# Performance work log

Hardware: AMD Instinct MI355X
Metric: run time of the kernel (lower is better)

The kernel has to match this reference:

```python
import jax, jax.numpy as jnp
import numpy as np


def _unfold(x, r):
    # x: [b, ch, h, w] -> [b, ch, k*k, h, w], zero-padded 3x3-style neighborhoods
    b, ch, h, w = x.shape
    k = 2 * r + 1
    xp = jnp.pad(x, ((0, 0), (0, 0), (r, r), (r, r)))
    patches = [xp[:, :, i:i + h, j:j + w] for i in range(k) for j in range(k)]
    return jnp.stack(patches, axis=2)


def setup_inputs() -> dict:
    key = jax.random.key(0)
    ks = jax.random.split(key, 6)
    b, c, h, w = 4, 128, 128, 128
    scale = 1.0 / np.sqrt(c)
    return {
        "feature0": jax.random.normal(ks[0], (b, c, h, w), jnp.float32),
        "flow": jax.random.normal(ks[1], (b, 2, h, w), jnp.float32),
        "q_w": jax.random.normal(ks[2], (c, c), jnp.float32) * scale,
        "q_b": jax.random.normal(ks[3], (c,), jnp.float32) * 0.01,
        "k_w": jax.random.normal(ks[4], (c, c), jnp.float32) * scale,
        "k_b": jax.random.normal(ks[5], (c,), jnp.float32) * 0.01,
        "local_window_attn": 1,
        "local_window_radius": 1,
    }


def reference(feature0, flow, q_w, q_b, k_w, k_b, local_window_attn, local_window_radius):
    b, c, h, w = feature0.shape
    inv_sqrt_c = 1.0 / jnp.sqrt(jnp.asarray(c, feature0.dtype))
    x = feature0.reshape(b, c, h * w).transpose(0, 2, 1)  # [b, hw, c]
    q = x @ q_w.T + q_b  # q_proj
    if local_window_attn:
        r = local_window_radius
        kf = x @ k_w.T + k_b  # k_proj applied to original feature
        kmap = kf.transpose(0, 2, 1).reshape(b, c, h, w)
        kwin = _unfold(kmap, r)      # [b, c, k2, h, w]
        fwin = _unfold(flow, r)      # [b, 2, k2, h, w]
        qmap = q.reshape(b, h, w, c)
        scores = jnp.einsum('bhwc,bckhw->bhwk', qmap, kwin) * inv_sqrt_c
        prob = jax.nn.softmax(scores, axis=-1)
        out = jnp.einsum('bhwk,bfkhw->bfhw', prob, fwin)  # [b, 2, h, w]
        return out
    else:
        # NOTE: faithful to source, key = k_proj(q_proj(x))
        key_ = q @ k_w.T + k_b
        value = flow.reshape(b, flow.shape[1], h * w).transpose(0, 2, 1)  # [b, hw, 2]
        scores = jnp.einsum('bnc,bmc->bnm', q, key_) * inv_sqrt_c
        prob = jax.nn.softmax(scores, axis=-1)
        out = jnp.einsum('bnm,bmf->bnf', prob, value)
        return out.reshape(b, h, w, value.shape[-1]).transpose(0, 3, 1, 2)
```

## Files before the change

### kernel.cpp

```cpp
#include <hip/hip_runtime.h>


#define HW 16384
#define NB 4
#define TOT (NB * HW)

typedef short bf16x8 __attribute__((ext_vector_type(8)));
typedef float f32x4 __attribute__((ext_vector_type(4)));

__device__ __forceinline__ unsigned short f2bf(float f) {
    unsigned u = __float_as_uint(f);
    return (unsigned short)((u + 0x7fffu + ((u >> 16) & 1u)) >> 16);
}
__device__ __forceinline__ float bf2f(unsigned short s) {
    return __uint_as_float(((unsigned)s) << 16);
}

__global__ void prep_kernel(const float* __restrict__ qw, const float* __restrict__ qb,
                            const float* __restrict__ kw, const float* __restrict__ kb,
                            unsigned short* __restrict__ Mh, unsigned short* __restrict__ Ml,
                            float* __restrict__ u, float* __restrict__ v,
                            float* __restrict__ dptr) {
    __shared__ float red[128];
    int bid = blockIdx.x, tid = threadIdx.x;
    if (bid < 16) {
        int ci = bid * 8 + (tid >> 5);
        int cj = (tid & 31) * 4;
        float4 acc = make_float4(0.f, 0.f, 0.f, 0.f);
#pragma unroll 4
        for (int co = 0; co < 128; ++co) {
            float qv = qw[co * 128 + ci];
            float4 kv = *(const float4*)(kw + co * 128 + cj);
            acc.x += qv * kv.x; acc.y += qv * kv.y;
            acc.z += qv * kv.z; acc.w += qv * kv.w;
        }
        int o = ci * 128 + cj;
        float a[4] = {acc.x, acc.y, acc.z, acc.w};
#pragma unroll
        for (int j = 0; j < 4; ++j) {
            unsigned short h = f2bf(a[j]);
            Mh[o + j] = h;
            Ml[o + j] = f2bf(a[j] - bf2f(h));
        }
    } else {
        int half = tid >> 7, t = tid & 127;
        const float* w  = half ? kw : qw;
        const float* bv = half ? qb : kb;
        float acc = 0.f;
#pragma unroll 4
        for (int co = 0; co < 128; ++co) acc += w[co * 128 + t] * bv[co];
        if (half) v[t] = acc; else u[t] = acc;
        if (!half) red[t] = qb[t] * kb[t];
        __syncthreads();
        if (tid == 0) {
            float dd = 0.f;
            for (int i = 0; i < 128; ++i) dd += red[i];
            *dptr = dd;
        }
    }
}

__global__ __launch_bounds__(256, 2)
void proj_kernel(const float* __restrict__ feat, const unsigned short* __restrict__ MhG,
                 const unsigned short* __restrict__ MlG, float* __restrict__ y) {
    int tid = threadIdx.x;
    int W = blockIdx.x * 4 + (tid >> 6);
    int lane = tid & 63;
    int cig = W & 3, pxg = W >> 2;
    int ci0 = cig * 32;
    int P0 = pxg * 64;
    int b = P0 >> 14, p0 = P0 & (HW - 1);
    int m = lane & 15, q = lane >> 4;
    const float* xbase = feat + (size_t)b * 128 * HW + p0;

    f32x4 zero = {0.f, 0.f, 0.f, 0.f};
    f32x4 acc[2][4];
#pragma unroll
    for (int t = 0; t < 2; ++t)
#pragma unroll
        for (int s = 0; s < 4; ++s) acc[t][s] = zero;

#pragma unroll
    for (int kc = 0; kc < 4; ++kc) {
        int c0 = kc * 32;
        bf16x8 ah[2], al[2];
#pragma unroll
        for (int t = 0; t < 2; ++t) {
            int roff = (ci0 + t * 16 + m) * 128 + c0 + q * 8;
            ah[t] = *(const bf16x8*)(MhG + roff);
            al[t] = *(const bf16x8*)(MlG + roff);
        }
        bf16x8 bh[4], bl[4];
#pragma unroll
        for (int s = 0; s < 4; ++s) {
            const float* xp = xbase + (size_t)(c0 + q * 8) * HW + s * 16 + m;
            float xv[8];
#pragma unroll
            for (int j = 0; j < 8; ++j) xv[j] = xp[(size_t)j * HW];
#pragma unroll
            for (int j = 0; j < 8; ++j) {
                unsigned short h = f2bf(xv[j]);
                bh[s][j] = (short)h;
                bl[s][j] = (short)f2bf(xv[j] - bf2f(h));
            }
        }
#pragma unroll
        for (int t = 0; t < 2; ++t)
#pragma unroll
            for (int s = 0; s < 4; ++s) {
                acc[t][s] = __builtin_amdgcn_mfma_f32_16x16x32_bf16(ah[t], bh[s], acc[t][s], 0, 0, 0);
                acc[t][s] = __builtin_amdgcn_mfma_f32_16x16x32_bf16(ah[t], bl[s], acc[t][s], 0, 0, 0);
                acc[t][s] = __builtin_amdgcn_mfma_f32_16x16x32_bf16(al[t], bh[s], acc[t][s], 0, 0, 0);
            }
    }

    int rg = lane >> 4, col = lane & 15;
#pragma unroll
    for (int t = 0; t < 2; ++t)
#pragma unroll
        for (int s = 0; s < 4; ++s) {
            float* yp = y + ((size_t)b * 128 + ci0 + t * 16 + rg * 4) * HW + p0 + s * 16 + col;
#pragma unroll
            for (int r = 0; r < 4; ++r) yp[(size_t)r * HW] = acc[t][s][r];
        }
}

__global__ __launch_bounds__(256, 4)
void attn_partial_kernel(const float* __restrict__ feat, const float* __restrict__ y,
                         const float* __restrict__ u, const float* __restrict__ v,
                         float* __restrict__ ps, float* __restrict__ gd) {
    int tid = threadIdx.x;
    int blk = blockIdx.x;
    int cg = blk >> 7;
    int pp = (blk & 127) * 256 + tid;
    int P = pp * 2;
    int b = P >> 14;
    int p = P & (HW - 1);
    const float* xb = feat + ((size_t)b * 128 + cg * 32) * HW + p;
    const float* yb = y + ((size_t)b * 128 + cg * 32) * HW + p;

    float s0[9], s1[9];
#pragma unroll
    for (int k = 0; k < 9; ++k) { s0[k] = 0.f; s1[k] = 0.f; }
    float g0 = 0.f, g1 = 0.f, d0 = 0.f, d1 = 0.f;

#pragma unroll 2
    for (int c = 0; c < 32; ++c) {
        float2 xv = *(const float2*)(xb + (size_t)c * HW);
        float uc = u[cg * 32 + c], vc = v[cg * 32 + c];
        g0 += xv.x * uc; g1 += xv.y * uc;
        d0 += xv.x * vc; d1 += xv.y * vc;
        const float* yc = yb + (size_t)c * HW;
#pragma unroll
        for (int dy = 0; dy < 3; ++dy) {
            const float* yr = yc + (dy - 1) * 128;
            float2 a  = *(const float2*)(yr - 2);
            float2 bb = *(const float2*)(yr);
            float2 cc = *(const float2*)(yr + 2);
            s0[dy * 3 + 0] += xv.x * a.y;   s1[dy * 3 + 0] += xv.y * bb.x;
            s0[dy * 3 + 1] += xv.x * bb.x;  s1[dy * 3 + 1] += xv.y * bb.y;
            s0[dy * 3 + 2] += xv.x * bb.y;  s1[dy * 3 + 2] += xv.y * cc.x;
        }
    }
    float* pso = ps + (size_t)cg * 9 * TOT + P;
#pragma unroll
    for (int k = 0; k < 9; ++k)
        *(float2*)(pso + (size_t)k * TOT) = make_float2(s0[k], s1[k]);
    *(float2*)(gd + (size_t)(cg * 2 + 0) * TOT + P) = make_float2(g0, g1);
    *(float2*)(gd + (size_t)(cg * 2 + 1) * TOT + P) = make_float2(d0, d1);
}

__global__ __launch_bounds__(256, 4)
void attn_final_kernel(const float* __restrict__ flow, const float* __restrict__ ps,
                       const float* __restrict__ gd, const float* __restrict__ dptr,
                       float* __restrict__ out) {
    int P = blockIdx.x * 256 + threadIdx.x;
    int b = P >> 14, p = P & (HW - 1);
    int row = p >> 7, col = p & 127;
    const float inv = 0.08838834764831845f;
    float dconst = *dptr;

    float g = 0.f;
#pragma unroll
    for (int cg = 0; cg < 4; ++cg) g += gd[(size_t)(cg * 2) * TOT + P];

    float sc[9];
    float mx = -1e30f;
#pragma unroll
    for (int k = 0; k < 9; ++k) {
        int dy = k / 3 - 1, dx = (k % 3) - 1;
        bool valid = ((unsigned)(row + dy) < 128u) && ((unsigned)(col + dx) < 128u);
        float ssum = 0.f;
#pragma unroll
        for (int cg = 0; cg < 4; ++cg) ssum += ps[(size_t)(cg * 9 + k) * TOT + P];
        int Pn = P + dy * 128 + dx;
        Pn = max(0, min(TOT - 1, Pn));
        float dsum = dconst;
#pragma unroll
        for (int cg = 0; cg < 4; ++cg) dsum += gd[(size_t)(cg * 2 + 1) * TOT + Pn];
        float s = valid ? (ssum + g + dsum) * inv : 0.f;
        sc[k] = s;
        mx = fmaxf(mx, s);
    }
    float e[9], sum = 0.f;
#pragma unroll
    for (int k = 0; k < 9; ++k) { e[k] = __expf(sc[k] - mx); sum += e[k]; }
    float rs = 1.f / sum;

    float o0 = 0.f, o1 = 0.f;
#pragma unroll
    for (int k = 0; k < 9; ++k) {
        int dy = k / 3 - 1, dx = (k % 3) - 1;
        bool valid = ((unsigned)(row + dy) < 128u) && ((unsigned)(col + dx) < 128u);
        float pr = valid ? e[k] * rs : 0.f;
        int fi0 = b * 2 * HW + p + dy * 128 + dx;
        fi0 = max(0, min(2 * TOT - 1, fi0));
        int fi1 = (b * 2 + 1) * HW + p + dy * 128 + dx;
        fi1 = max(0, min(2 * TOT - 1, fi1));
        o0 += pr * flow[fi0];
        o1 += pr * flow[fi1];
    }
    out[(size_t)(b * 2) * HW + p] = o0;
    out[(size_t)(b * 2 + 1) * HW + p] = o1;
}

extern "C" void kernel_launch(void* const* d_in, const int* in_sizes, int n_in,
                              void* d_out, int out_size, void* d_ws, size_t ws_size,
                              hipStream_t stream) {
    const float* feat = (const float*)d_in[0];
    const float* flow = (const float*)d_in[1];
    const float* qw = (const float*)d_in[2];
    const float* qb = (const float*)d_in[3];
    const float* kw = (const float*)d_in[4];
    const float* kb = (const float*)d_in[5];

    float* ws = (float*)d_ws;
    float* u = ws;
    float* v = ws + 128;
    float* dptr = ws + 256;
    unsigned short* Mh = (unsigned short*)(ws + 512);
    unsigned short* Ml = (unsigned short*)(ws + 8704);
    float* y = ws + 16896;
    float* ps = ws + 8405760;
    float* gd = ws + 10765056;
    float* out = (float*)d_out;

    prep_kernel<<<17, 256, 0, stream>>>(qw, qb, kw, kb, Mh, Ml, u, v, dptr);
    proj_kernel<<<1024, 256, 0, stream>>>(feat, Mh, Ml, y);
    attn_partial_kernel<<<512, 256, 0, stream>>>(feat, y, u, v, ps, gd);
    attn_final_kernel<<<256, 256, 0, stream>>>(flow, ps, gd, dptr, out);
}
```

Measured before the change: 127.4 us.

## Fuse gamma/delta bias dot products into projection kernel and widen partial attention

Measured after the change: 138.6 us. 8.8% more time.

```diff
diff --git a/kernel.cpp b/kernel.cpp
--- a/kernel.cpp
+++ b/kernel.cpp
@@ -62,12 +62,15 @@
 
 __global__ __launch_bounds__(256, 2)
 void proj_kernel(const float* __restrict__ feat, const unsigned short* __restrict__ MhG,
-                 const unsigned short* __restrict__ MlG, float* __restrict__ y) {
+                 const unsigned short* __restrict__ MlG,
+                 const float* __restrict__ u, const float* __restrict__ v,
+                 const float* __restrict__ dptr, float* __restrict__ y,
+                 float* __restrict__ gam, float* __restrict__ del) {
     int tid = threadIdx.x;
-    int W = blockIdx.x * 4 + (tid >> 6);
     int lane = tid & 63;
-    int cig = W & 3, pxg = W >> 2;
+    int cig = tid >> 6;
     int ci0 = cig * 32;
+    int pxg = blockIdx.x;
     int P0 = pxg * 64;
     int b = P0 >> 14, p0 = P0 & (HW - 1);
     int m = lane & 15, q = lane >> 4;
@@ -79,6 +82,8 @@
     for (int t = 0; t < 2; ++t)
 #pragma unroll
         for (int s = 0; s < 4; ++s) acc[t][s] = zero;
+    float gacc[4] = {0.f, 0.f, 0.f, 0.f};
+    float dacc[4] = {0.f, 0.f, 0.f, 0.f};
 
 #pragma unroll
     for (int kc = 0; kc < 4; ++kc) {
@@ -90,6 +95,14 @@
             ah[t] = *(const bf16x8*)(MhG + roff);
             al[t] = *(const bf16x8*)(MlG + roff);
         }
+        float uj[8], vj[8];
+        if (cig == 0) {
+#pragma unroll
+            for (int j = 0; j < 8; ++j) {
+                uj[j] = u[c0 + q * 8 + j];
+                vj[j] = v[c0 + q * 8 + j];
+            }
+        }
         bf16x8 bh[4], bl[4];
 #pragma unroll
         for (int s = 0; s < 4; ++s) {
@@ -97,6 +110,13 @@
             float xv[8];
 #pragma unroll
             for (int j = 0; j < 8; ++j) xv[j] = xp[(size_t)j * HW];
+            if (cig == 0) {
+#pragma unroll
+                for (int j = 0; j < 8; ++j) {
+                    gacc[s] = fmaf(xv[j], uj[j], gacc[s]);
+                    dacc[s] = fmaf(xv[j], vj[j], dacc[s]);
+                }
+            }
 #pragma unroll
             for (int j = 0; j < 8; ++j) {
                 unsigned short h = f2bf(xv[j]);
@@ -114,6 +134,20 @@
             }
     }
 
+    if (cig == 0) {
+        float dconst = *dptr;
+#pragma unroll
+        for (int s = 0; s < 4; ++s) {
+            float g = gacc[s], dd = dacc[s];
+            g += __shfl_xor(g, 16);  g += __shfl_xor(g, 32);
+            dd += __shfl_xor(dd, 16); dd += __shfl_xor(dd, 32);
+            if (q == 0) {
+                gam[(size_t)b * HW + p0 + s * 16 + m] = g;
+                del[(size_t)b * HW + p0 + s * 16 + m] = dd + dconst;
+            }
+        }
+    }
+
     int rg = lane >> 4, col = lane & 15;
 #pragma unroll
     for (int t = 0; t < 2; ++t)
@@ -127,63 +161,55 @@
 
 __global__ __launch_bounds__(256, 4)
 void attn_partial_kernel(const float* __restrict__ feat, const float* __restrict__ y,
-                         const float* __restrict__ u, const float* __restrict__ v,
-                         float* __restrict__ ps, float* __restrict__ gd) {
+                         float* __restrict__ ps) {
     int tid = threadIdx.x;
     int blk = blockIdx.x;
-    int cg = blk >> 7;
-    int pp = (blk & 127) * 256 + tid;
-    int P = pp * 2;
+    int cg = blk >> 6;
+    int P = ((blk & 63) * 256 + tid) * 4;
     int b = P >> 14;
     int p = P & (HW - 1);
     const float* xb = feat + ((size_t)b * 128 + cg * 32) * HW + p;
     const float* yb = y + ((size_t)b * 128 + cg * 32) * HW + p;
 
-    float s0[9], s1[9];
-#pragma unroll
-    for (int k = 0; k < 9; ++k) { s0[k] = 0.f; s1[k] = 0.f; }
-    float g0 = 0.f, g1 = 0.f, d0 = 0.f, d1 = 0.f;
+    f32x4 s[9];
+#pragma unroll
+    for (int k = 0; k < 9; ++k) s[k] = (f32x4){0.f, 0.f, 0.f, 0.f};
 
 #pragma unroll 2
     for (int c = 0; c < 32; ++c) {
-        float2 xv = *(const float2*)(xb + (size_t)c * HW);
-        float uc = u[cg * 32 + c], vc = v[cg * 32 + c];
-        g0 += xv.x * uc; g1 += xv.y * uc;
-        d0 += xv.x * vc; d1 += xv.y * vc;
+        float4 xv = *(const float4*)(xb + (size_t)c * HW);
         const float* yc = yb + (size_t)c * HW;
 #pragma unroll
         for (int dy = 0; dy < 3; ++dy) {
             const float* yr = yc + (dy - 1) * 128;
-            float2 a  = *(const float2*)(yr - 2);
-            float2 bb = *(const float2*)(yr);
-            float2 cc = *(const float2*)(yr + 2);
-            s0[dy * 3 + 0] += xv.x * a.y;   s1[dy * 3 + 0] += xv.y * bb.x;
-            s0[dy * 3 + 1] += xv.x * bb.x;  s1[dy * 3 + 1] += xv.y * bb.y;
-            s0[dy * 3 + 2] += xv.x * bb.y;  s1[dy * 3 + 2] += xv.y * cc.x;
+            float4 mm = *(const float4*)(yr);
+            float lm = yr[-1];
+            float rp = yr[4];
+            int k = dy * 3;
+            s[k][0] += xv.x * lm;    s[k][1] += xv.y * mm.x;
+            s[k][2] += xv.z * mm.y;  s[k][3] += xv.w * mm.z;
+            s[k+1][0] += xv.x * mm.x; s[k+1][1] += xv.y * mm.y;
+            s[k+1][2] += xv.z * mm.z; s[k+1][3] += xv.w * mm.w;
+            s[k+2][0] += xv.x * mm.y; s[k+2][1] += xv.y * mm.z;
+            s[k+2][2] += xv.z * mm.w; s[k+2][3] += xv.w * rp;
         }
     }
     float* pso = ps + (size_t)cg * 9 * TOT + P;
 #pragma unroll
     for (int k = 0; k < 9; ++k)
-        *(float2*)(pso + (size_t)k * TOT) = make_float2(s0[k], s1[k]);
-    *(float2*)(gd + (size_t)(cg * 2 + 0) * TOT + P) = make_float2(g0, g1);
-    *(float2*)(gd + (size_t)(cg * 2 + 1) * TOT + P) = make_float2(d0, d1);
+        *(f32x4*)(pso + (size_t)k * TOT) = s[k];
 }
 
 __global__ __launch_bounds__(256, 4)
 void attn_final_kernel(const float* __restrict__ flow, const float* __restrict__ ps,
-                       const float* __restrict__ gd, const float* __restrict__ dptr,
+                       const float* __restrict__ gam, const float* __restrict__ del,
                        float* __restrict__ out) {
     int P = blockIdx.x * 256 + threadIdx.x;
     int b = P >> 14, p = P & (HW - 1);
     int row = p >> 7, col = p & 127;
     const float inv = 0.08838834764831845f;
-    float dconst = *dptr;
-
-    float g = 0.f;
-#pragma unroll
-    for (int cg = 0; cg < 4; ++cg) g += gd[(size_t)(cg * 2) * TOT + P];
-
+
+    float g = gam[P];
     float sc[9];
     float mx = -1e30f;
 #pragma unroll
@@ -195,10 +221,7 @@
         for (int cg = 0; cg < 4; ++cg) ssum += ps[(size_t)(cg * 9 + k) * TOT + P];
         int Pn = P + dy * 128 + dx;
         Pn = max(0, min(TOT - 1, Pn));
-        float dsum = dconst;
-#pragma unroll
-        for (int cg = 0; cg < 4; ++cg) dsum += gd[(size_t)(cg * 2 + 1) * TOT + Pn];
-        float s = valid ? (ssum + g + dsum) * inv : 0.f;
+        float s = valid ? (ssum + g + del[Pn]) * inv : 0.f;
         sc[k] = s;
         mx = fmaxf(mx, s);
     }
@@ -242,11 +265,12 @@
     unsigned short* Ml = (unsigned short*)(ws + 8704);
     float* y = ws + 16896;
     float* ps = ws + 8405760;
-    float* gd = ws + 10765056;
+    float* gam = ws + 10765056;
+    float* del = ws + 10830592;
     float* out = (float*)d_out;
 
     prep_kernel<<<17, 256, 0, stream>>>(qw, qb, kw, kb, Mh, Ml, u, v, dptr);
-    proj_kernel<<<1024, 256, 0, stream>>>(feat, Mh, Ml, y);
-    attn_partial_kernel<<<512, 256, 0, stream>>>(feat, y, u, v, ps, gd);
-    attn_final_kernel<<<256, 256, 0, stream>>>(flow, ps, gd, dptr, out);
-}
+    proj_kernel<<<1024, 256, 0, stream>>>(feat, Mh, Ml, u, v, dptr, y, gam, del);
+    attn_partial_kernel<<<256, 256, 0, stream>>>(feat, y, ps);
+    attn_final_kernel<<<256, 256, 0, stream>>>(flow, ps, gam, del, out);
+}
```
